# Kernel optimization log

Measured on AMD Instinct MI355X. Metric: run time of the kernel, lower is better.

The kernel has to match this reference:

```python
import jax, jax.numpy as jnp
import numpy as np

D_MODEL = 768
N_HEADS = 12
D_FF = 3072
EPS = 1e-5


def _dense_params(key, d_in, d_out):
    kw, kb = jax.random.split(key)
    bound = 1.0 / np.sqrt(d_in)
    W = jax.random.uniform(kw, (d_in, d_out), minval=-bound, maxval=bound, dtype=jnp.float32)
    b = jax.random.uniform(kb, (d_out,), minval=-bound, maxval=bound, dtype=jnp.float32)
    return W, b


def setup_inputs() -> dict:
    key = jax.random.key(0)
    ks = jax.random.split(key, 8)
    x = jax.random.normal(ks[0], (2, 2048, D_MODEL), dtype=jnp.float32)
    wq, bq = _dense_params(ks[1], D_MODEL, D_MODEL)
    wk, bk = _dense_params(ks[2], D_MODEL, D_MODEL)
    wv, bv = _dense_params(ks[3], D_MODEL, D_MODEL)
    wo, bo = _dense_params(ks[4], D_MODEL, D_MODEL)
    w1, b1 = _dense_params(ks[5], D_MODEL, D_FF)
    w2, b2 = _dense_params(ks[6], D_FF, D_MODEL)
    g1 = jnp.ones((D_MODEL,), jnp.float32); be1 = jnp.zeros((D_MODEL,), jnp.float32)
    g2 = jnp.ones((D_MODEL,), jnp.float32); be2 = jnp.zeros((D_MODEL,), jnp.float32)
    return {"x": x, "wq": wq, "bq": bq, "wk": wk, "bk": bk, "wv": wv, "bv": bv,
            "wo": wo, "bo": bo, "w1": w1, "b1": b1, "w2": w2, "b2": b2,
            "g1": g1, "be1": be1, "g2": g2, "be2": be2}


def _layernorm(x, g, b):
    mu = jnp.mean(x, axis=-1, keepdims=True)
    var = jnp.mean(jnp.square(x - mu), axis=-1, keepdims=True)
    return (x - mu) * jax.lax.rsqrt(var + EPS) * g + b


def reference(x, wq, bq, wk, bk, wv, bv, wo, bo, w1, b1, w2, b2, g1, be1, g2, be2):
    B, S, D = x.shape
    H, dk = N_HEADS, D // N_HEADS
    # projections -> [B, H, S, dk]
    def split_heads(t):
        return t.reshape(B, S, H, dk).transpose(0, 2, 1, 3)
    q = split_heads(x @ wq + bq)
    k = split_heads(x @ wk + bk)
    v = split_heads(x @ wv + bv)
    scores = jnp.einsum('bhqd,bhkd->bhqk', q, k) / np.sqrt(dk).astype(np.float32)
    causal = jnp.tril(jnp.ones((S, S), dtype=bool))  # True = keep
    scores = jnp.where(causal, scores, -jnp.inf)
    attn = jax.nn.softmax(scores, axis=-1)
    out = jnp.einsum('bhqk,bhkd->bhqd', attn, v)
    out = out.transpose(0, 2, 1, 3).reshape(B, S, D)
    attn_out = out @ wo + bo
    x = _layernorm(x + attn_out, g1, be1)
    ff = jax.nn.relu(x @ w1 + b1) @ w2 + b2
    x = _layernorm(x + ff, g2, be2)
    return x
```

## Files before the change

kernel.cpp:

```cpp
#include <hip/hip_runtime.h>
#include <stdint.h>

#define S_LEN 2048
#define BATCH 2
#define DM 768
#define NH 12
#define DKH 64
#define DFF 3072
#define MROWS (BATCH * S_LEN)
#define NBH (BATCH * NH)

typedef short bf16x8 __attribute__((ext_vector_type(8)));
typedef float f32x4 __attribute__((ext_vector_type(4)));
typedef float f32x16 __attribute__((ext_vector_type(16)));

__device__ __forceinline__ unsigned short f2b(float f) {
    union { float f; unsigned u; } cv; cv.f = f;
    unsigned u = cv.u;
    unsigned r = (u + 0x7FFFu + ((u >> 16) & 1u)) >> 16;
    return (unsigned short)r;
}

__device__ __forceinline__ float b2f(unsigned short u) {
    union { unsigned u; float f; } cv; cv.u = ((unsigned)u) << 16;
    return cv.f;
}

__device__ __forceinline__ void gload16(const void* g, void* l) {
    __builtin_amdgcn_global_load_lds(
        (const __attribute__((address_space(1))) unsigned int*)g,
        (__attribute__((address_space(3))) unsigned int*)l, 16, 0, 0);
}

__device__ __forceinline__ unsigned cvtpk(float lo, float hi) {
    unsigned r;
    asm("v_cvt_pk_bf16_f32 %0, %1, %2" : "=v"(r) : "v"(lo), "v"(hi));
    return r;
}
__device__ __forceinline__ void pswap(unsigned &a, unsigned &b) {
    asm("v_permlane32_swap_b32 %0, %1" : "+v"(a), "+v"(b));
}
__device__ __forceinline__ bf16x8 mkpa(unsigned w0, unsigned w1, unsigned w2, unsigned w3) {
    union { unsigned u[4]; bf16x8 h; } cv;
    cv.u[0] = w0; cv.u[1] = w1; cv.u[2] = w2; cv.u[3] = w3;
    return cv.h;
}

__global__ __launch_bounds__(256) void prep_kernel(
    const float* __restrict__ x,
    const float* __restrict__ wq, const float* __restrict__ wk,
    const float* __restrict__ wv, const float* __restrict__ wo,
    const float* __restrict__ w1, const float* __restrict__ w2,
    unsigned short* __restrict__ x16, unsigned short* __restrict__ wqkv16,
    unsigned short* __restrict__ wo16, unsigned short* __restrict__ w116,
    unsigned short* __restrict__ w216) {
    const int t = threadIdx.x;
    int bid = blockIdx.x;
    if (bid < 3072) {
        const int i = bid * 256 + t;
        float4 v = reinterpret_cast<const float4*>(x)[i];
        ushort4 o;
        o.x = f2b(v.x); o.y = f2b(v.y); o.z = f2b(v.z); o.w = f2b(v.w);
        reinterpret_cast<ushort4*>(x16)[i] = o;
        return;
    }
    bid -= 3072;
    const float* in; unsigned short* out; int R, C, bx, by;
    if (bid < 2304) {
        const int wsel = bid / 576, r = bid % 576;
        in = (wsel == 0) ? wq : (wsel == 1) ? wk : (wsel == 2) ? wv : wo;
        out = (wsel == 3) ? wo16 : wqkv16 + (size_t)wsel * DM * DM;
        R = DM; C = DM; bx = r % 24; by = r / 24;
    } else if (bid < 4608) {
        const int r = bid - 2304;
        in = w1; out = w116; R = DM; C = DFF; bx = r % 96; by = r / 96;
    } else {
        const int r = bid - 4608;
        in = w2; out = w216; R = DFF; C = DM; bx = r % 24; by = r / 24;
    }
    __shared__ float tile[32][33];
    const int c0 = bx * 32, r0 = by * 32;
    const int tx = t & 31, ty = t >> 5;
    #pragma unroll
    for (int i = ty; i < 32; i += 8)
        tile[i][tx] = in[(size_t)(r0 + i) * C + c0 + tx];
    __syncthreads();
    #pragma unroll
    for (int i = ty; i < 32; i += 8)
        out[(size_t)(c0 + i) * R + r0 + tx] = f2b(tile[tx][i]);
}

#define STG192(buf, kt)                                                                  \
    {                                                                                    \
        const char* ga = (const char*)(A + (size_t)bm * lda + koff + ((kt) << 6));       \
        const char* gb = (const char*)(Bt + (size_t)bn * ldb + koff + ((kt) << 6));      \
        char* la = (char*)Sh + (buf) * 57344 + t * 16;                                   \
        char* lb = (char*)Sh + (buf) * 57344 + 32768 + t * 16;                           \
        _Pragma("unroll")                                                                \
        for (int p = 0; p < 4; ++p)                                                      \
            gload16(ga + (size_t)(sr + p * 64) * la2 + scb_sw, la + p * 8192);           \
        _Pragma("unroll")                                                                \
        for (int p = 0; p < 3; ++p)                                                      \
            gload16(gb + (size_t)(sr + p * 64) * lb2 + scb_sw, lb + p * 8192);           \
    }

template <int EPI>
__global__ __launch_bounds__(512, 2) void gemm192(
    const unsigned short* __restrict__ A, int lda,
    const unsigned short* __restrict__ Bt, int ldb,
    const float* __restrict__ bias0, const float* __restrict__ bias1,
    const float* __restrict__ bias2,
    unsigned short* __restrict__ ob0, unsigned short* __restrict__ ob1,
    unsigned short* __restrict__ ob2, float* __restrict__ of,
    int M, int N, int Ksub, float qscale) {
    __shared__ __align__(16) unsigned short Sh[2 * 28672];
    const int t = threadIdx.x;
    const int wave = t >> 6, lane = t & 63;
    const int wr = wave >> 2, wc = wave & 3;
    const int gx = gridDim.x;
    const int nl = gx * gridDim.y;
    const int lid = blockIdx.y * gx + blockIdx.x;
    const int logical = (lid & 7) * (nl >> 3) + (lid >> 3);
    const int bn = (logical % gx) * 192, bm = (logical / gx) * 256;
    const int koff = (EPI == 3) ? blockIdx.z * Ksub : 0;
    const int lr = lane & 15;
    const int lk8 = (lane >> 4) << 3;
    const int sr = t >> 3;
    const int scb = (t & 7) * 16;
    const int scb_sw = scb ^ ((sr & 7) << 4);
    const int swr = (lr & 7) << 4;
    const size_t la2 = (size_t)lda * 2, lb2 = (size_t)ldb * 2;

    f32x4 acc[8][3];
    #pragma unroll
    for (int i = 0; i < 8; ++i)
        #pragma unroll
        for (int j = 0; j < 3; ++j) { f32x4 z = {0.f, 0.f, 0.f, 0.f}; acc[i][j] = z; }

    const int nkt = Ksub >> 6;
    STG192(0, 0)
    for (int kt = 0; kt < nkt; ++kt) {
        const int cur = kt & 1;
        if (kt + 1 < nkt) {
            STG192(cur ^ 1, kt + 1)
            asm volatile("s_waitcnt vmcnt(7)" ::: "memory");
        } else {
            asm volatile("s_waitcnt vmcnt(0)" ::: "memory");
        }
        __builtin_amdgcn_s_barrier();
        __builtin_amdgcn_sched_barrier(0);
        const char* Ab = (const char*)Sh + cur * 57344;
        const char* Bb = Ab + 32768;
        #pragma unroll
        for (int ks = 0; ks < 64; ks += 32) {
            const int cbsw = ((ks + lk8) * 2) ^ swr;
            bf16x8 af[8], bfv[3];
            #pragma unroll
            for (int i = 0; i < 8; ++i)
                af[i] = *reinterpret_cast<const bf16x8*>(Ab + (wr * 128 + i * 16 + lr) * 128 + cbsw);
            #pragma unroll
            for (int j = 0; j < 3; ++j)
                bfv[j] = *reinterpret_cast<const bf16x8*>(Bb + (wc * 48 + j * 16 + lr) * 128 + cbsw);
            __builtin_amdgcn_s_setprio(1);
            #pragma unroll
            for (int i = 0; i < 8; ++i)
                #pragma unroll
                for (int j = 0; j < 3; ++j)
                    acc[i][j] = __builtin_amdgcn_mfma_f32_16x16x32_bf16(af[i], bfv[j], acc[i][j], 0, 0, 0);
            __builtin_amdgcn_s_setprio(0);
        }
        __builtin_amdgcn_s_barrier();
    }

    const int r0 = (lane >> 4) << 2;
    if (EPI == 0) {
        #pragma unroll
        for (int i = 0; i < 8; ++i) {
            const int row_b = bm + wr * 128 + i * 16 + r0;
            #pragma unroll
            for (int j = 0; j < 3; ++j) {
                const int col = bn + wc * 48 + j * 16 + lr;
                const float bvv = bias0[col];
                #pragma unroll
                for (int r = 0; r < 4; ++r) {
                    float vv = acc[i][j][r] + bvv;
                    vv = vv > 0.f ? vv : 0.f;
                    ob0[(size_t)(row_b + r) * N + col] = f2b(vv);
                }
            }
        }
    } else if (EPI == 1) {
        const int sec = (bn >= 2 * DM) ? 2 : (bn >= DM ? 1 : 0);
        const int nb = bn - sec * DM;
        const float* bias = (sec == 0) ? bias0 : (sec == 1 ? bias1 : bias2);
        #pragma unroll
        for (int i = 0; i < 8; ++i) {
            const int row_b = bm + wr * 128 + i * 16 + r0;
            const int b = row_b >> 11, s = row_b & 2047;
            #pragma unroll
            for (int j = 0; j < 3; ++j) {
                const int c768 = nb + wc * 48 + j * 16 + lr;
                const int h = c768 >> 6, d = c768 & 63;
                const float bvv = bias[c768];
                if (sec == 2) {
                    ushort4 w;
                    w.x = f2b(acc[i][j][0] + bvv);
                    w.y = f2b(acc[i][j][1] + bvv);
                    w.z = f2b(acc[i][j][2] + bvv);
                    w.w = f2b(acc[i][j][3] + bvv);
                    *reinterpret_cast<ushort4*>(
                        ob2 + (((size_t)(b * NH + h) * DKH) + d) * S_LEN + s) = w;
                } else {
                    const float sc = (sec == 0) ? qscale : 1.f;
                    unsigned short* dst = (sec == 0) ? ob0 : ob1;
                    #pragma unroll
                    for (int r = 0; r < 4; ++r)
                        dst[(((size_t)(b * NH + h) * S_LEN) + s + r) * DKH + d] =
                            f2b((acc[i][j][r] + bvv) * sc);
                }
            }
        }
    } else {
        unsigned short* op = ob0 + (size_t)blockIdx.z * M * N;
        #pragma unroll
        for (int i = 0; i < 8; ++i) {
            const int row_b = bm + wr * 128 + i * 16 + r0;
            #pragma unroll
            for (int j = 0; j < 3; ++j) {
                const int col = bn + wc * 48 + j * 16 + lr;
                #pragma unroll
                for (int r = 0; r < 4; ++r)
                    op[(size_t)(row_b + r) * N + col] = f2b(acc[i][j][r]);
            }
        }
    }
}

#define STAGEKV(buf, kt)                                                              \
    {                                                                                 \
        const char* kg = kbyte + (((size_t)(kt)) << 13);                              \
        const char* vg = vbyte + (((size_t)(kt)) << 7);                               \
        char* lk = (char*)&KV[buf][0][0] + lane * 16;                                 \
        char* lv = (char*)&KV[buf][1][0] + lane * 16;                                 \
        _Pragma("unroll")                                                             \
        for (int i = 0; i < 8; ++i)                                                   \
            gload16(kg + (i * 8 + sub) * 128 + ccs, lk + i * 1024);                   \
        _Pragma("unroll")                                                             \
        for (int i = 0; i < 8; ++i)                                                   \
            gload16(vg + (size_t)(i * 8 + sub) * (S_LEN * 2) + ccs, lv + i * 1024);   \
    }

__global__ __launch_bounds__(64) void attn_mfma_kernel(
    const unsigned short* __restrict__ q16,
    const unsigned short* __restrict__ k16,
    const unsigned short* __restrict__ vt16,
    unsigned short* __restrict__ ctx16) {
    __shared__ __align__(16) char KV[2][2][8192];
    const int lane = threadIdx.x & 63;
    const int bh = blockIdx.x;
    const int qb = (gridDim.y - 1) - blockIdx.y;
    const int b = bh / NH, h = bh % NH;
    const size_t hbase = (size_t)bh * S_LEN * DKH;
    const int x = lane & 31;
    const int hi = lane >> 5;
    const int k8 = hi << 3;
    const int sW = qb << 5;
    const int qg = sW + x;
    const int sub = lane >> 3;
    const int ccs = ((lane & 7) * 16) ^ (sub << 4);
    const int swz = (x & 7) << 4;

    bf16x8 qa[4];
    #pragma unroll
    for (int c = 0; c < 4; ++c)
        qa[c] = *reinterpret_cast<const bf16x8*>(
            q16 + hbase + (size_t)(sW + x) * DKH + c * 16 + k8);

    float mst = -3e38f, lst = 0.f;
    f32x16 acc0, acc1;
    #pragma unroll
    for (int r = 0; r < 16; ++r) { acc0[r] = 0.f; acc1[r] = 0.f; }

    const char* kbyte = (const char*)(k16 + hbase);
    const char* vbyte = (const char*)(vt16 + hbase);
    const int nt = (sW >> 6) + 1;

    STAGEKV(0, 0)
    for (int kt = 0; kt < nt; ++kt) {
        const int cur = kt & 1;
        asm volatile("s_waitcnt vmcnt(0)" ::: "memory");
        if (kt + 1 < nt) STAGEKV(cur ^ 1, kt + 1)
        const char* Kb = (const char*)&KV[cur][0][0];
        const char* Vb = (const char*)&KV[cur][1][0];
        const int k0 = kt << 6;

        bf16x8 kaf[2][4];
        #pragma unroll
        for (int kh = 0; kh < 2; ++kh)
            #pragma unroll
            for (int c = 0; c < 4; ++c)
                kaf[kh][c] = *reinterpret_cast<const bf16x8*>(
                    Kb + (kh * 32 + x) * 128 + ((c * 32 + hi * 16) ^ swz));

        f32x16 sc0, sc1;
        #pragma unroll
        for (int r = 0; r < 16; ++r) { sc0[r] = 0.f; sc1[r] = 0.f; }
        __builtin_amdgcn_s_setprio(1);
        #pragma unroll
        for (int c = 0; c < 4; ++c) {
            sc0 = __builtin_amdgcn_mfma_f32_32x32x16_bf16(kaf[0][c], qa[c], sc0, 0, 0, 0);
            sc1 = __builtin_amdgcn_mfma_f32_32x32x16_bf16(kaf[1][c], qa[c], sc1, 0, 0, 0);
        }
        __builtin_amdgcn_s_setprio(0);

        if (kt == nt - 1) {
            #pragma unroll
            for (int r = 0; r < 16; ++r) {
                const int cr = (r & 3) + (hi << 2) + ((r >> 2) << 3);
                if (k0 + cr > qg) sc0[r] = -3e38f;
                if (k0 + 32 + cr > qg) sc1[r] = -3e38f;
            }
        }

        float tm = fmaxf(sc0[0], sc0[1]);
        #pragma unroll
        for (int r = 2; r < 16; ++r) tm = fmaxf(tm, sc0[r]);
        #pragma unroll
        for (int r = 0; r < 16; ++r) tm = fmaxf(tm, sc1[r]);
        tm = fmaxf(tm, __shfl_xor(tm, 32));

        if (!__all(tm <= mst + 8.f)) {
            const float mn = fmaxf(mst, tm);
            const float corr = exp2f(mst - mn);
            mst = mn;
            lst *= corr;
            float cw[16];
            #pragma unroll
            for (int r = 0; r < 16; ++r)
                cw[r] = __shfl(corr, (r & 3) + (hi << 2) + ((r >> 2) << 3));
            #pragma unroll
            for (int r = 0; r < 16; ++r) { acc0[r] *= cw[r]; acc1[r] *= cw[r]; }
        }

        float ts = 0.f;
        #pragma unroll
        for (int r = 0; r < 16; ++r) {
            sc0[r] = exp2f(sc0[r] - mst); ts += sc0[r];
            sc1[r] = exp2f(sc1[r] - mst); ts += sc1[r];
        }
        ts += __shfl_xor(ts, 32);
        lst += ts;

        unsigned a0 = cvtpk(sc0[0], sc0[1]),   b0 = cvtpk(sc0[4], sc0[5]);   pswap(a0, b0);
        unsigned a1 = cvtpk(sc0[2], sc0[3]),   b1 = cvtpk(sc0[6], sc0[7]);   pswap(a1, b1);
        unsigned a2 = cvtpk(sc0[8], sc0[9]),   b2 = cvtpk(sc0[12], sc0[13]); pswap(a2, b2);
        unsigned a3 = cvtpk(sc0[10], sc0[11]), b3 = cvtpk(sc0[14], sc0[15]); pswap(a3, b3);
        bf16x8 pa00 = mkpa(a0, a1, b0, b1);
        bf16x8 pa01 = mkpa(a2, a3, b2, b3);
        unsigned c0 = cvtpk(sc1[0], sc1[1]),   d0 = cvtpk(sc1[4], sc1[5]);   pswap(c0, d0);
        unsigned c1 = cvtpk(sc1[2], sc1[3]),   d1 = cvtpk(sc1[6], sc1[7]);   pswap(c1, d1);
        unsigned c2 = cvtpk(sc1[8], sc1[9]),   d2 = cvtpk(sc1[12], sc1[13]); pswap(c2, d2);
        unsigned c3 = cvtpk(sc1[10], sc1[11]), d3 = cvtpk(sc1[14], sc1[15]); pswap(c3, d3);
        bf16x8 pa10 = mkpa(c0, c1, d0, d1);
        bf16x8 pa11 = mkpa(c2, c3, d2, d3);

        bf16x8 vaf[2][4];
        #pragma unroll
        for (int dt = 0; dt < 2; ++dt)
            #pragma unroll
            for (int s = 0; s < 4; ++s)
                vaf[dt][s] = *reinterpret_cast<const bf16x8*>(
                    Vb + (dt * 32 + x) * 128 + ((s * 32 + hi * 16) ^ swz));

        __builtin_amdgcn_s_setprio(1);
        acc0 = __builtin_amdgcn_mfma_f32_32x32x16_bf16(pa00, vaf[0][0], acc0, 0, 0, 0);
        acc1 = __builtin_amdgcn_mfma_f32_32x32x16_bf16(pa00, vaf[1][0], acc1, 0, 0, 0);
        acc0 = __builtin_amdgcn_mfma_f32_32x32x16_bf16(pa01, vaf[0][1], acc0, 0, 0, 0);
        acc1 = __builtin_amdgcn_mfma_f32_32x32x16_bf16(pa01, vaf[1][1], acc1, 0, 0, 0);
        acc0 = __builtin_amdgcn_mfma_f32_32x32x16_bf16(pa10, vaf[0][2], acc0, 0, 0, 0);
        acc1 = __builtin_amdgcn_mfma_f32_32x32x16_bf16(pa10, vaf[1][2], acc1, 0, 0, 0);
        acc0 = __builtin_amdgcn_mfma_f32_32x32x16_bf16(pa11, vaf[0][3], acc0, 0, 0, 0);
        acc1 = __builtin_amdgcn_mfma_f32_32x32x16_bf16(pa11, vaf[1][3], acc1, 0, 0, 0);
        __builtin_amdgcn_s_setprio(0);
    }

    const float li = 1.f / lst;
    float lw[16];
    #pragma unroll
    for (int r = 0; r < 16; ++r)
        lw[r] = __shfl(li, (r & 3) + (hi << 2) + ((r >> 2) << 3));
    #pragma unroll
    for (int r = 0; r < 16; ++r) {
        const int q = sW + (r & 3) + (hi << 2) + ((r >> 2) << 3);
        const size_t rowb = ((size_t)b * S_LEN + q) * DM + h * DKH;
        ctx16[rowb + x] = f2b(acc0[r] * lw[r]);
        ctx16[rowb + 32 + x] = f2b(acc1[r] * lw[r]);
    }
}

template <int EB16>
__global__ __launch_bounds__(192) void ln_merge_kernel(
    const unsigned short* __restrict__ part, size_t pstride, int ns,
    const float* __restrict__ res, const float* __restrict__ bias,
    const float* __restrict__ gam, const float* __restrict__ bet,
    float* __restrict__ outf, unsigned short* __restrict__ outb) {
    __shared__ float red[8];
    const int row = blockIdx.x, t = threadIdx.x;
    const int wave = t >> 6, lane = t & 63;
    const size_t base = (size_t)row * DM;
    float4 v = reinterpret_cast<const float4*>(res + base)[t];
    const float4 bv = reinterpret_cast<const float4*>(bias)[t];
    v.x += bv.x; v.y += bv.y; v.z += bv.z; v.w += bv.w;
    for (int z = 0; z < ns; ++z) {
        const ushort4 p = reinterpret_cast<const ushort4*>(part + (size_t)z * pstride + base)[t];
        v.x += b2f(p.x); v.y += b2f(p.y); v.z += b2f(p.z); v.w += b2f(p.w);
    }
    float s = v.x + v.y + v.z + v.w;
    float sq = v.x * v.x + v.y * v.y + v.z * v.z + v.w * v.w;
    #pragma unroll
    for (int off = 32; off > 0; off >>= 1) { s += __shfl_xor(s, off); sq += __shfl_xor(sq, off); }
    if (lane == 0) { red[wave] = s; red[wave + 4] = sq; }
    __syncthreads();
    s = red[0] + red[1] + red[2];
    sq = red[4] + red[5] + red[6];
    const float mu = s * (1.f / DM);
    const float var = sq * (1.f / DM) - mu * mu;
    const float rs = rsqrtf(var + 1e-5f);
    const float4 g = reinterpret_cast<const float4*>(gam)[t];
    const float4 be = reinterpret_cast<const float4*>(bet)[t];
    float4 o;
    o.x = (v.x - mu) * rs * g.x + be.x;
    o.y = (v.y - mu) * rs * g.y + be.y;
    o.z = (v.z - mu) * rs * g.z + be.z;
    o.w = (v.w - mu) * rs * g.w + be.w;
    reinterpret_cast<float4*>(outf + base)[t] = o;
    if (EB16) {
        ushort4 ob;
        ob.x = f2b(o.x); ob.y = f2b(o.y); ob.z = f2b(o.z); ob.w = f2b(o.w);
        reinterpret_cast<ushort4*>(outb + base)[t] = ob;
    }
}

extern "C" void kernel_launch(void* const* d_in, const int* in_sizes, int n_in,
                              void* d_out, int out_size, void* d_ws, size_t ws_size,
                              hipStream_t stream) {
    const float* x   = (const float*)d_in[0];
    const float* wq  = (const float*)d_in[1];
    const float* bq  = (const float*)d_in[2];
    const float* wk  = (const float*)d_in[3];
    const float* bk  = (const float*)d_in[4];
    const float* wv  = (const float*)d_in[5];
    const float* bv  = (const float*)d_in[6];
    const float* wo  = (const float*)d_in[7];
    const float* bo  = (const float*)d_in[8];
    const float* w1  = (const float*)d_in[9];
    const float* b1  = (const float*)d_in[10];
    const float* w2  = (const float*)d_in[11];
    const float* b2  = (const float*)d_in[12];
    const float* g1  = (const float*)d_in[13];
    const float* be1 = (const float*)d_in[14];
    const float* g2  = (const float*)d_in[15];
    const float* be2 = (const float*)d_in[16];

    char* wp = (char*)d_ws;
    auto alloc = [&](size_t bytes) -> void* {
        void* r = (void*)wp;
        wp += (bytes + 255) & ~(size_t)255;
        return r;
    };
    const int M = MROWS;
    unsigned short* wqkv16 = (unsigned short*)alloc((size_t)3 * DM * DM * 2);
    unsigned short* wo16 = (unsigned short*)alloc((size_t)DM * DM * 2);
    unsigned short* w116 = (unsigned short*)alloc((size_t)DM * DFF * 2);
    unsigned short* w216 = (unsigned short*)alloc((size_t)DM * DFF * 2);
    unsigned short* ctx16 = (unsigned short*)alloc((size_t)M * DM * 2);
    float* y1 = (float*)alloc((size_t)M * DM * 4);
    unsigned short* x16  = (unsigned short*)alloc((size_t)M * DM * 2);
    unsigned short* q16  = (unsigned short*)alloc((size_t)M * DM * 2);
    unsigned short* k16  = (unsigned short*)alloc((size_t)M * DM * 2);
    unsigned short* vt16 = (unsigned short*)alloc((size_t)M * DM * 2);
    unsigned short* ff116 = x16;
    unsigned short* x116  = ctx16;

    const size_t perb = (size_t)M * DM * 2;
    size_t used = (size_t)(wp - (char*)d_ws);
    int NS = 1;
    if (used + 4 * perb + 1024 <= ws_size) NS = 4;
    else if (used + 2 * perb + 1024 <= ws_size) NS = 2;
    unsigned short* part = (unsigned short*)alloc((size_t)NS * perb);
    const int NSW = (NS >= 2) ? 2 : 1;

    prep_kernel<<<9984, 256, 0, stream>>>(x, wq, wk, wv, wo, w1, w2,
                                          x16, wqkv16, wo16, w116, w216);

    const float QSCALE = 0.125f * 1.44269504088896f;
    gemm192<1><<<dim3(3 * DM / 192, M / 256), 512, 0, stream>>>(
        x16, DM, wqkv16, DM, bq, bk, bv, q16, k16, vt16, nullptr, M, 3 * DM, DM, QSCALE);

    attn_mfma_kernel<<<dim3(NBH, S_LEN / 32), 64, 0, stream>>>(q16, k16, vt16, ctx16);

    gemm192<3><<<dim3(DM / 192, M / 256, NSW), 512, 0, stream>>>(
        ctx16, DM, wo16, DM, nullptr, nullptr, nullptr, part, nullptr, nullptr, nullptr,
        M, DM, DM / NSW, 1.f);
    ln_merge_kernel<1><<<M, 192, 0, stream>>>(part, (size_t)M * DM, NSW, x, bo, g1, be1, y1, x116);

    gemm192<0><<<dim3(DFF / 192, M / 256), 512, 0, stream>>>(
        x116, DM, w116, DM, b1, nullptr, nullptr, ff116, nullptr, nullptr, nullptr, M, DFF, DM, 1.f);

    gemm192<3><<<dim3(DM / 192, M / 256, NS), 512, 0, stream>>>(
        ff116, DFF, w216, DFF, nullptr, nullptr, nullptr, part, nullptr, nullptr, nullptr,
        M, DM, DFF / NS, 1.f);
    ln_merge_kernel<0><<<M, 192, 0, stream>>>(part, (size_t)M * DM, NS, y1, b2, g2, be2,
                                              (float*)d_out, nullptr);
}
```

Before: 174.4 us.

## Double attention KV tile to 128 keys and drop fp32 LN residual buffer

The attention kernel now stages 128 keys per iteration, with 32KB of K and V per buffer, and computes four 32-key score blocks before the PV MFMAs. This halves loop iterations and wait points but doubles LDS use, which may reduce occupancy and adds masked work on the diagonal tile. The second layernorm now reads its residual from the bf16 copy of the first layernorm output instead of a separate fp32 buffer. That removes one fp32 write and read, at the cost of reduced residual precision.

```diff
diff --git a/kernel.cpp b/kernel.cpp
--- a/kernel.cpp
+++ b/kernel.cpp
@@ -44,6 +44,22 @@
     union { unsigned u[4]; bf16x8 h; } cv;
     cv.u[0] = w0; cv.u[1] = w1; cv.u[2] = w2; cv.u[3] = w3;
     return cv.h;
+}
+
+__device__ __forceinline__ float vmax16(const f32x16& v) {
+    float a0 = fmaxf(v[0], v[1]), a1 = fmaxf(v[2], v[3]);
+    float a2 = fmaxf(v[4], v[5]), a3 = fmaxf(v[6], v[7]);
+    float a4 = fmaxf(v[8], v[9]), a5 = fmaxf(v[10], v[11]);
+    float a6 = fmaxf(v[12], v[13]), a7 = fmaxf(v[14], v[15]);
+    float b0 = fmaxf(a0, a1), b1 = fmaxf(a2, a3);
+    float b2 = fmaxf(a4, a5), b3 = fmaxf(a6, a7);
+    return fmaxf(fmaxf(b0, b1), fmaxf(b2, b3));
+}
+__device__ __forceinline__ float vsum16(const f32x16& v) {
+    float a0 = v[0] + v[1], a1 = v[2] + v[3], a2 = v[4] + v[5], a3 = v[6] + v[7];
+    float a4 = v[8] + v[9], a5 = v[10] + v[11], a6 = v[12] + v[13], a7 = v[14] + v[15];
+    float b0 = a0 + a1, b1 = a2 + a3, b2 = a4 + a5, b3 = a6 + a7;
+    return (b0 + b1) + (b2 + b3);
 }
 
 __global__ __launch_bounds__(256) void prep_kernel(
@@ -236,18 +252,23 @@
     }
 }
 
-#define STAGEKV(buf, kt)                                                              \
-    {                                                                                 \
-        const char* kg = kbyte + (((size_t)(kt)) << 13);                              \
-        const char* vg = vbyte + (((size_t)(kt)) << 7);                               \
-        char* lk = (char*)&KV[buf][0][0] + lane * 16;                                 \
-        char* lv = (char*)&KV[buf][1][0] + lane * 16;                                 \
-        _Pragma("unroll")                                                             \
-        for (int i = 0; i < 8; ++i)                                                   \
-            gload16(kg + (i * 8 + sub) * 128 + ccs, lk + i * 1024);                   \
-        _Pragma("unroll")                                                             \
-        for (int i = 0; i < 8; ++i)                                                   \
-            gload16(vg + (size_t)(i * 8 + sub) * (S_LEN * 2) + ccs, lv + i * 1024);   \
+#define STAGEKV(buf, kt)                                                                   \
+    {                                                                                      \
+        const char* kg = kbyte + (((size_t)(kt)) << 14);                                   \
+        const char* vg = vbyte + (((size_t)(kt)) << 8);                                    \
+        char* bb = (char*)KV + (buf) * 32768;                                              \
+        char* lk = bb + lane * 16;                                                         \
+        char* lv0 = bb + 16384 + lane * 16;                                                \
+        char* lv1 = bb + 24576 + lane * 16;                                                \
+        _Pragma("unroll")                                                                  \
+        for (int i = 0; i < 16; ++i)                                                       \
+            gload16(kg + (i * 8 + sub) * 128 + ccs, lk + i * 1024);                        \
+        _Pragma("unroll")                                                                  \
+        for (int i = 0; i < 8; ++i)                                                        \
+            gload16(vg + (size_t)(i * 8 + sub) * (S_LEN * 2) + ccs, lv0 + i * 1024);       \
+        _Pragma("unroll")                                                                  \
+        for (int i = 0; i < 8; ++i)                                                        \
+            gload16(vg + 128 + (size_t)(i * 8 + sub) * (S_LEN * 2) + ccs, lv1 + i * 1024); \
     }
 
 __global__ __launch_bounds__(64) void attn_mfma_kernel(
@@ -255,7 +276,7 @@
     const unsigned short* __restrict__ k16,
     const unsigned short* __restrict__ vt16,
     unsigned short* __restrict__ ctx16) {
-    __shared__ __align__(16) char KV[2][2][8192];
+    __shared__ __align__(16) char KV[2 * 32768];
     const int lane = threadIdx.x & 63;
     const int bh = blockIdx.x;
     const int qb = (gridDim.y - 1) - blockIdx.y;
@@ -283,50 +304,49 @@
 
     const char* kbyte = (const char*)(k16 + hbase);
     const char* vbyte = (const char*)(vt16 + hbase);
-    const int nt = (sW >> 6) + 1;
+    const int nt = (sW >> 7) + 1;
 
     STAGEKV(0, 0)
     for (int kt = 0; kt < nt; ++kt) {
         const int cur = kt & 1;
         asm volatile("s_waitcnt vmcnt(0)" ::: "memory");
         if (kt + 1 < nt) STAGEKV(cur ^ 1, kt + 1)
-        const char* Kb = (const char*)&KV[cur][0][0];
-        const char* Vb = (const char*)&KV[cur][1][0];
-        const int k0 = kt << 6;
-
-        bf16x8 kaf[2][4];
-        #pragma unroll
-        for (int kh = 0; kh < 2; ++kh)
+        const char* Kb = (const char*)KV + cur * 32768;
+        const char* Vb0 = Kb + 16384;
+        const char* Vb1 = Kb + 24576;
+        const int k0 = kt << 7;
+
+        f32x16 sc[4];
+        #pragma unroll
+        for (int hh = 0; hh < 4; ++hh)
+            #pragma unroll
+            for (int r = 0; r < 16; ++r) sc[hh][r] = 0.f;
+        __builtin_amdgcn_s_setprio(1);
+        #pragma unroll
+        for (int hh = 0; hh < 4; ++hh) {
+            bf16x8 kaf[4];
             #pragma unroll
             for (int c = 0; c < 4; ++c)
-                kaf[kh][c] = *reinterpret_cast<const bf16x8*>(
-                    Kb + (kh * 32 + x) * 128 + ((c * 32 + hi * 16) ^ swz));
-
-        f32x16 sc0, sc1;
-        #pragma unroll
-        for (int r = 0; r < 16; ++r) { sc0[r] = 0.f; sc1[r] = 0.f; }
-        __builtin_amdgcn_s_setprio(1);
-        #pragma unroll
-        for (int c = 0; c < 4; ++c) {
-            sc0 = __builtin_amdgcn_mfma_f32_32x32x16_bf16(kaf[0][c], qa[c], sc0, 0, 0, 0);
-            sc1 = __builtin_amdgcn_mfma_f32_32x32x16_bf16(kaf[1][c], qa[c], sc1, 0, 0, 0);
+                kaf[c] = *reinterpret_cast<const bf16x8*>(
+                    Kb + (hh * 32 + x) * 128 + ((c * 32 + hi * 16) ^ swz));
+            #pragma unroll
+            for (int c = 0; c < 4; ++c)
+                sc[hh] = __builtin_amdgcn_mfma_f32_32x32x16_bf16(kaf[c], qa[c], sc[hh], 0, 0, 0);
         }
         __builtin_amdgcn_s_setprio(0);
 
         if (kt == nt - 1) {
             #pragma unroll
-            for (int r = 0; r < 16; ++r) {
-                const int cr = (r & 3) + (hi << 2) + ((r >> 2) << 3);
-                if (k0 + cr > qg) sc0[r] = -3e38f;
-                if (k0 + 32 + cr > qg) sc1[r] = -3e38f;
-            }
-        }
-
-        float tm = fmaxf(sc0[0], sc0[1]);
-        #pragma unroll
-        for (int r = 2; r < 16; ++r) tm = fmaxf(tm, sc0[r]);
-        #pragma unroll
-        for (int r = 0; r < 16; ++r) tm = fmaxf(tm, sc1[r]);
+            for (int hh = 0; hh < 4; ++hh)
+                #pragma unroll
+                for (int r = 0; r < 16; ++r) {
+                    const int cr = (r & 3) + (hi << 2) + ((r >> 2) << 3);
+                    if (k0 + hh * 32 + cr > qg) sc[hh][r] = -3e38f;
+                }
+        }
+
+        float tm = fmaxf(fmaxf(vmax16(sc[0]), vmax16(sc[1])),
+                         fmaxf(vmax16(sc[2]), vmax16(sc[3])));
         tm = fmaxf(tm, __shfl_xor(tm, 32));
 
         if (!__all(tm <= mst + 8.f)) {
@@ -342,45 +362,37 @@
             for (int r = 0; r < 16; ++r) { acc0[r] *= cw[r]; acc1[r] *= cw[r]; }
         }
 
-        float ts = 0.f;
-        #pragma unroll
-        for (int r = 0; r < 16; ++r) {
-            sc0[r] = exp2f(sc0[r] - mst); ts += sc0[r];
-            sc1[r] = exp2f(sc1[r] - mst); ts += sc1[r];
-        }
+        #pragma unroll
+        for (int hh = 0; hh < 4; ++hh)
+            #pragma unroll
+            for (int r = 0; r < 16; ++r) sc[hh][r] = exp2f(sc[hh][r] - mst);
+        float ts = (vsum16(sc[0]) + vsum16(sc[1])) + (vsum16(sc[2]) + vsum16(sc[3]));
         ts += __shfl_xor(ts, 32);
         lst += ts;
 
-        unsigned a0 = cvtpk(sc0[0], sc0[1]),   b0 = cvtpk(sc0[4], sc0[5]);   pswap(a0, b0);
-        unsigned a1 = cvtpk(sc0[2], sc0[3]),   b1 = cvtpk(sc0[6], sc0[7]);   pswap(a1, b1);
-        unsigned a2 = cvtpk(sc0[8], sc0[9]),   b2 = cvtpk(sc0[12], sc0[13]); pswap(a2, b2);
-        unsigned a3 = cvtpk(sc0[10], sc0[11]), b3 = cvtpk(sc0[14], sc0[15]); pswap(a3, b3);
-        bf16x8 pa00 = mkpa(a0, a1, b0, b1);
-        bf16x8 pa01 = mkpa(a2, a3, b2, b3);
-        unsigned c0 = cvtpk(sc1[0], sc1[1]),   d0 = cvtpk(sc1[4], sc1[5]);   pswap(c0, d0);
-        unsigned c1 = cvtpk(sc1[2], sc1[3]),   d1 = cvtpk(sc1[6], sc1[7]);   pswap(c1, d1);
-        unsigned c2 = cvtpk(sc1[8], sc1[9]),   d2 = cvtpk(sc1[12], sc1[13]); pswap(c2, d2);
-        unsigned c3 = cvtpk(sc1[10], sc1[11]), d3 = cvtpk(sc1[14], sc1[15]); pswap(c3, d3);
-        bf16x8 pa10 = mkpa(c0, c1, d0, d1);
-        bf16x8 pa11 = mkpa(c2, c3, d2, d3);
-
-        bf16x8 vaf[2][4];
-        #pragma unroll
-        for (int dt = 0; dt < 2; ++dt)
-            #pragma unroll
-            for (int s = 0; s < 4; ++s)
-                vaf[dt][s] = *reinterpret_cast<const bf16x8*>(
-                    Vb + (dt * 32 + x) * 128 + ((s * 32 + hi * 16) ^ swz));
+        bf16x8 pa[8];
+        #pragma unroll
+        for (int hh = 0; hh < 4; ++hh) {
+            unsigned a0 = cvtpk(sc[hh][0], sc[hh][1]),   b0 = cvtpk(sc[hh][4], sc[hh][5]);   pswap(a0, b0);
+            unsigned a1 = cvtpk(sc[hh][2], sc[hh][3]),   b1 = cvtpk(sc[hh][6], sc[hh][7]);   pswap(a1, b1);
+            unsigned a2 = cvtpk(sc[hh][8], sc[hh][9]),   b2 = cvtpk(sc[hh][12], sc[hh][13]); pswap(a2, b2);
+            unsigned a3 = cvtpk(sc[hh][10], sc[hh][11]), b3 = cvtpk(sc[hh][14], sc[hh][15]); pswap(a3, b3);
+            pa[hh * 2] = mkpa(a0, a1, b0, b1);
+            pa[hh * 2 + 1] = mkpa(a2, a3, b2, b3);
+        }
 
         __builtin_amdgcn_s_setprio(1);
-        acc0 = __builtin_amdgcn_mfma_f32_32x32x16_bf16(pa00, vaf[0][0], acc0, 0, 0, 0);
-        acc1 = __builtin_amdgcn_mfma_f32_32x32x16_bf16(pa00, vaf[1][0], acc1, 0, 0, 0);
-        acc0 = __builtin_amdgcn_mfma_f32_32x32x16_bf16(pa01, vaf[0][1], acc0, 0, 0, 0);
-        acc1 = __builtin_amdgcn_mfma_f32_32x32x16_bf16(pa01, vaf[1][1], acc1, 0, 0, 0);
-        acc0 = __builtin_amdgcn_mfma_f32_32x32x16_bf16(pa10, vaf[0][2], acc0, 0, 0, 0);
-        acc1 = __builtin_amdgcn_mfma_f32_32x32x16_bf16(pa10, vaf[1][2], acc1, 0, 0, 0);
-        acc0 = __builtin_amdgcn_mfma_f32_32x32x16_bf16(pa11, vaf[0][3], acc0, 0, 0, 0);
-        acc1 = __builtin_amdgcn_mfma_f32_32x32x16_bf16(pa11, vaf[1][3], acc1, 0, 0, 0);
+        #pragma unroll
+        for (int s = 0; s < 8; ++s) {
+            const char* Vh = (s < 4) ? Vb0 : Vb1;
+            const int so = s & 3;
+            bf16x8 v0 = *reinterpret_cast<const bf16x8*>(
+                Vh + (0 * 32 + x) * 128 + ((so * 32 + hi * 16) ^ swz));
+            bf16x8 v1 = *reinterpret_cast<const bf16x8*>(
+                Vh + (1 * 32 + x) * 128 + ((so * 32 + hi * 16) ^ swz));
+            acc0 = __builtin_amdgcn_mfma_f32_32x32x16_bf16(pa[s], v0, acc0, 0, 0, 0);
+            acc1 = __builtin_amdgcn_mfma_f32_32x32x16_bf16(pa[s], v1, acc1, 0, 0, 0);
+        }
         __builtin_amdgcn_s_setprio(0);
     }
 
@@ -398,17 +410,23 @@
     }
 }
 
-template <int EB16>
+template <int EB16OUT, int RES16>
 __global__ __launch_bounds__(192) void ln_merge_kernel(
     const unsigned short* __restrict__ part, size_t pstride, int ns,
-    const float* __restrict__ res, const float* __restrict__ bias,
+    const void* __restrict__ res, const float* __restrict__ bias,
     const float* __restrict__ gam, const float* __restrict__ bet,
     float* __restrict__ outf, unsigned short* __restrict__ outb) {
     __shared__ float red[8];
     const int row = blockIdx.x, t = threadIdx.x;
     const int wave = t >> 6, lane = t & 63;
     const size_t base = (size_t)row * DM;
-    float4 v = reinterpret_cast<const float4*>(res + base)[t];
+    float4 v;
+    if (RES16) {
+        const ushort4 rv = reinterpret_cast<const ushort4*>((const unsigned short*)res + base)[t];
+        v.x = b2f(rv.x); v.y = b2f(rv.y); v.z = b2f(rv.z); v.w = b2f(rv.w);
+    } else {
+        v = reinterpret_cast<const float4*>((const float*)res + base)[t];
+    }
     const float4 bv = reinterpret_cast<const float4*>(bias)[t];
     v.x += bv.x; v.y += bv.y; v.z += bv.z; v.w += bv.w;
     for (int z = 0; z < ns; ++z) {
@@ -433,11 +451,12 @@
     o.y = (v.y - mu) * rs * g.y + be.y;
     o.z = (v.z - mu) * rs * g.z + be.z;
     o.w = (v.w - mu) * rs * g.w + be.w;
-    reinterpret_cast<float4*>(outf + base)[t] = o;
-    if (EB16) {
+    if (EB16OUT) {
         ushort4 ob;
         ob.x = f2b(o.x); ob.y = f2b(o.y); ob.z = f2b(o.z); ob.w = f2b(o.w);
         reinterpret_cast<ushort4*>(outb + base)[t] = ob;
+    } else {
+        reinterpret_cast<float4*>(outf + base)[t] = o;
     }
 }
 
@@ -474,7 +493,6 @@
     unsigned short* w116 = (unsigned short*)alloc((size_t)DM * DFF * 2);
     unsigned short* w216 = (unsigned short*)alloc((size_t)DM * DFF * 2);
     unsigned short* ctx16 = (unsigned short*)alloc((size_t)M * DM * 2);
-    float* y1 = (float*)alloc((size_t)M * DM * 4);
     unsigned short* x16  = (unsigned short*)alloc((size_t)M * DM * 2);
     unsigned short* q16  = (unsigned short*)alloc((size_t)M * DM * 2);
     unsigned short* k16  = (unsigned short*)alloc((size_t)M * DM * 2);
@@ -502,7 +520,8 @@
     gemm192<3><<<dim3(DM / 192, M / 256, NSW), 512, 0, stream>>>(
         ctx16, DM, wo16, DM, nullptr, nullptr, nullptr, part, nullptr, nullptr, nullptr,
         M, DM, DM / NSW, 1.f);
-    ln_merge_kernel<1><<<M, 192, 0, stream>>>(part, (size_t)M * DM, NSW, x, bo, g1, be1, y1, x116);
+    ln_merge_kernel<1, 0><<<M, 192, 0, stream>>>(part, (size_t)M * DM, NSW, x, bo, g1, be1,
+                                                 nullptr, x116);
 
     gemm192<0><<<dim3(DFF / 192, M / 256), 512, 0, stream>>>(
         x116, DM, w116, DM, b1, nullptr, nullptr, ff116, nullptr, nullptr, nullptr, M, DFF, DM, 1.f);
@@ -510,6 +529,6 @@
     gemm192<3><<<dim3(DM / 192, M / 256, NS), 512, 0, stream>>>(
         ff116, DFF, w216, DFF, nullptr, nullptr, nullptr, part, nullptr, nullptr, nullptr,
         M, DM, DFF / NS, 1.f);
-    ln_merge_kernel<0><<<M, 192, 0, stream>>>(part, (size_t)M * DM, NS, y1, b2, g2, be2,
-                                              (float*)d_out, nullptr);
-}
+    ln_merge_kernel<0, 1><<<M, 192, 0, stream>>>(part, (size_t)M * DM, NS, x116, b2, g2, be2,
+                                                 (float*)d_out, nullptr);
+}
```

Result: slower. 212.9 us (+22.1%).
